# Kernel optimization log

Hardware: AMD Instinct MI355X
Metric: run time of the kernel (lower is better)

## Reference

```python
import jax, jax.numpy as jnp
import numpy as np

EPS = 1e-6
H, HKV, D = 32, 8, 64          # heads, kv heads, head_dim
E, TOP_K, FF = 8, 2, 1024      # experts, top-k, expert intermediate
HID = 2048


def rms_norm(x, w):
    xf = x.astype(jnp.float32)
    var = jnp.mean(xf * xf, axis=-1, keepdims=True)
    return (w * (xf * jax.lax.rsqrt(var + EPS)).astype(x.dtype))


def rotate_half(x):
    x1, x2 = jnp.split(x, 2, axis=-1)
    return jnp.concatenate([-x2, x1], axis=-1)


def apply_rope(q, k, cos, sin):
    # cos/sin: [B,S,rd] -> [B,1,S,rd]
    cos = cos[:, None, :, :]
    sin = sin[:, None, :, :]
    rd = cos.shape[-1]
    q_rot, q_pass = q[..., :rd], q[..., rd:]
    k_rot, k_pass = k[..., :rd], k[..., rd:]
    q_emb = q_rot * cos + rotate_half(q_rot) * sin
    k_emb = k_rot * cos + rotate_half(k_rot) * sin
    return (jnp.concatenate([q_emb, q_pass], -1), jnp.concatenate([k_emb, k_pass], -1))


def attention(x, cos, sin, wq, wk, wv, wo):
    B, S, _ = x.shape
    q = (x @ wq).reshape(B, S, H, D).transpose(0, 2, 1, 3)      # [B,H,S,D]
    k = (x @ wk).reshape(B, S, HKV, D).transpose(0, 2, 1, 3)    # [B,Hk,S,D]
    v = (x @ wv).reshape(B, S, HKV, D).transpose(0, 2, 1, 3)
    q, k = apply_rope(q, k, cos, sin)
    rep = H // HKV
    k = jnp.repeat(k, rep, axis=1)
    v = jnp.repeat(v, rep, axis=1)
    scale = D ** -0.5
    scores = jnp.einsum('bhqd,bhkd->bhqk', q, k) * scale
    causal = jnp.triu(jnp.full((S, S), -jnp.inf, dtype=scores.dtype), k=1)
    scores = scores + causal
    probs = jax.nn.softmax(scores.astype(jnp.float32), axis=-1).astype(q.dtype)
    out = jnp.einsum('bhqk,bhkd->bhqd', probs, v)
    out = out.transpose(0, 2, 1, 3).reshape(B, S, H * D)
    return out @ wo


def moe(x, gate_w, corr_bias, w1, w2, w3):
    B, S, Dm = x.shape
    xf = x.reshape(-1, Dm)                                      # [T, Dm]
    T = xf.shape[0]
    logits = xf @ gate_w                                        # [T, E]
    rw = jax.nn.sigmoid(logits.astype(jnp.float32))
    scores = rw + corr_bias
    _, sel = jax.lax.top_k(scores, TOP_K)                       # [T, k]
    tw = jnp.take_along_axis(rw, sel, axis=-1)
    tw = tw / jnp.sum(tw, axis=-1, keepdims=True)
    # dense [T, E] combine weights (zero for unselected experts)
    cw = jnp.zeros((T, E), dtype=xf.dtype).at[jnp.arange(T)[:, None], sel].set(tw.astype(xf.dtype))
    # run every expert densely, combine with sparse weights (same math as gather/scatter loop)
    h = jax.nn.silu(jnp.einsum('td,edf->etf', xf, w1)) * jnp.einsum('td,edf->etf', xf, w3)
    eo = jnp.einsum('etf,efd->etd', h, w2)                      # [E, T, Dm]
    out = jnp.einsum('etd,te->td', eo, cw)
    return out.reshape(B, S, Dm)


def setup_inputs() -> dict:
    key = jax.random.key(0)
    ks = jax.random.split(key, 16)
    s = 0.02
    return {
        'hidden_states': jax.random.normal(ks[0], (2, 1024, HID), jnp.float32),
        'cos': jax.random.uniform(ks[1], (2, 1024, D), jnp.float32),
        'sin': jax.random.uniform(ks[2], (2, 1024, D), jnp.float32),
        'ln1_w': jnp.ones((HID,), jnp.float32),
        'ln2_w': jnp.ones((HID,), jnp.float32),
        'wq': jax.random.normal(ks[3], (HID, H * D), jnp.float32) * s,
        'wk': jax.random.normal(ks[4], (HID, HKV * D), jnp.float32) * s,
        'wv': jax.random.normal(ks[5], (HID, HKV * D), jnp.float32) * s,
        'wo': jax.random.normal(ks[6], (H * D, HID), jnp.float32) * s,
        'gate_w': jax.random.normal(ks[7], (HID, E), jnp.float32) * s,
        'corr_bias': jnp.zeros((E,), jnp.float32),
        'w1': jax.random.normal(ks[8], (E, HID, FF), jnp.float32) * s,
        'w2': jax.random.normal(ks[9], (E, FF, HID), jnp.float32) * s,
        'w3': jax.random.normal(ks[10], (E, HID, FF), jnp.float32) * s,
    }


def reference(hidden_states, cos, sin, ln1_w, ln2_w, wq, wk, wv, wo, gate_w, corr_bias, w1, w2, w3):
    residual = hidden_states
    h = rms_norm(hidden_states, ln1_w)
    h = attention(h, cos, sin, wq, wk, wv, wo)
    h = residual + h
    residual = h
    h = rms_norm(h, ln2_w)
    h = moe(h, gate_w, corr_bias, w1, w2, w3)
    return residual + h
```

## Files before the change

kernel.cpp:

```cpp
#include <hip/hip_runtime.h>
#include <hip/hip_bf16.h>

#define DEV static __device__ __forceinline__

typedef __attribute__((ext_vector_type(8))) short short8;
typedef __attribute__((ext_vector_type(8))) __bf16 bf16x8;
typedef __attribute__((ext_vector_type(4))) float floatx4;

DEV short f2bf(float f) {
  unsigned u = __builtin_bit_cast(unsigned, f);
  unsigned r = (u + 0x7fffu + ((u >> 16) & 1u)) >> 16;
  return (short)(unsigned short)r;
}
DEV float bf2f(short s) {
  unsigned u = ((unsigned)(unsigned short)s) << 16;
  return __builtin_bit_cast(float, u);
}
DEV floatx4 mfma16(short8 a, short8 b, floatx4 c) {
  return __builtin_amdgcn_mfma_f32_16x16x32_bf16(
      __builtin_bit_cast(bf16x8, a), __builtin_bit_cast(bf16x8, b), c, 0, 0, 0);
}

DEV int sw2(int r) { return (r ^ (r >> 2)) & 3; }

DEV const short* sbase(const short* src, int ld, int row0, int id) {
  int r = id >> 2, cc = id & 3;
  return src + (long)(row0 + r) * ld + ((cc ^ sw2(r)) << 3);
}
DEV void sissue(short* ldsbuf, const short* base, int k0, int tid, int slotbase) {
  int wave = tid >> 6;
  __builtin_amdgcn_global_load_lds(
      (const __attribute__((address_space(1))) void*)(base + k0),
      (__attribute__((address_space(3))) void*)(ldsbuf + (slotbase + wave * 64) * 8),
      16, 0, 0);
}
DEV short8 rdfrag(const short* lds, int row, int l4) {
  return *(const short8*)(lds + row * 32 + ((l4 ^ sw2(row)) << 3));
}

DEV const short* sb64(const short* src, int ld, int row0, int id) {
  int r = id >> 3, c = id & 7;
  return src + (long)(row0 + r) * ld + ((c ^ (r & 7)) << 3);
}
DEV const short* sb64g(const short* src, int ld, const int* rows, int p0, int plim,
                       int id) {
  int r = id >> 3, c = id & 7;
  int pi = p0 + r;
  if (pi > plim) pi = plim;
  return src + (long)rows[pi] * ld + ((c ^ (r & 7)) << 3);
}
DEV short8 rd64(const short* lds, int row, int ch) {
  return *(const short8*)(lds + row * 64 + ((ch ^ (row & 7)) << 3));
}

__global__ __launch_bounds__(256) void k_gemm_qkv(
    const short* Ah, const short* Al, const short* Bh, const short* Bl,
    short* qbh, short* qbl, short* kbh, short* kbl, short* vbh, short* vbl,
    const float* cs, const float* sn) {
  const int K = 2048;
  __shared__ __align__(16) short AsH[2][4096], AsL[2][4096], BsH[2][4096], BsL[2][4096];
  int tid = threadIdx.x, lane = tid & 63, wave = tid >> 6;
  int l15 = lane & 15, l4 = lane >> 4;
  int wm = wave >> 1, wn = wave & 1;
  int bid = blockIdx.y * 24 + blockIdx.x;
  int swz = (bid & 7) * 48 + (bid >> 3);
  int bx = swz % 24, by = swz / 24;
  int m0 = by * 128, n0 = bx * 128;

  const short* bAH0 = sbase(Ah, K, m0, tid);
  const short* bAH1 = sbase(Ah, K, m0, tid + 256);
  const short* bAL0 = sbase(Al, K, m0, tid);
  const short* bAL1 = sbase(Al, K, m0, tid + 256);
  const short* bBH0 = sbase(Bh, K, n0, tid);
  const short* bBH1 = sbase(Bh, K, n0, tid + 256);
  const short* bBL0 = sbase(Bl, K, n0, tid);
  const short* bBL1 = sbase(Bl, K, n0, tid + 256);

  auto STAGE = [&](int buf, int k0) {
    sissue(AsH[buf], bAH0, k0, tid, 0);
    sissue(AsH[buf], bAH1, k0, tid, 256);
    sissue(AsL[buf], bAL0, k0, tid, 0);
    sissue(AsL[buf], bAL1, k0, tid, 256);
    sissue(BsH[buf], bBH0, k0, tid, 0);
    sissue(BsH[buf], bBH1, k0, tid, 256);
    sissue(BsL[buf], bBL0, k0, tid, 0);
    sissue(BsL[buf], bBL1, k0, tid, 256);
  };

  floatx4 zero4 = {0.f, 0.f, 0.f, 0.f};
  floatx4 acc[4][4];
#pragma unroll
  for (int i = 0; i < 4; ++i)
#pragma unroll
    for (int j = 0; j < 4; ++j) acc[i][j] = zero4;

  STAGE(0, 0);
  __syncthreads();
  int cur = 0;
  for (int k0 = 0; k0 < K; k0 += 32) {
    if (k0 + 32 < K) STAGE(cur ^ 1, k0 + 32);
    short8 ah[4], al[4], bh2[4], bl2[4];
#pragma unroll
    for (int mi = 0; mi < 4; ++mi) {
      ah[mi] = rdfrag(AsH[cur], wm * 64 + mi * 16 + l15, l4);
      al[mi] = rdfrag(AsL[cur], wm * 64 + mi * 16 + l15, l4);
    }
#pragma unroll
    for (int nt = 0; nt < 4; ++nt) {
      bh2[nt] = rdfrag(BsH[cur], wn * 64 + nt * 16 + l15, l4);
      bl2[nt] = rdfrag(BsL[cur], wn * 64 + nt * 16 + l15, l4);
    }
#pragma unroll
    for (int mi = 0; mi < 4; ++mi)
#pragma unroll
      for (int nt = 0; nt < 4; ++nt) {
        acc[mi][nt] = mfma16(al[mi], bh2[nt], acc[mi][nt]);
        acc[mi][nt] = mfma16(ah[mi], bl2[nt], acc[mi][nt]);
        acc[mi][nt] = mfma16(ah[mi], bh2[nt], acc[mi][nt]);
      }
    __syncthreads();
    cur ^= 1;
  }

  int hb = n0 + wn * 64;
  bool isq = hb < 2048, isk = (!isq) && hb < 2560;
  if (isq || isk) {
#pragma unroll
    for (int mi = 0; mi < 4; ++mi)
#pragma unroll
      for (int ntp = 0; ntp < 2; ++ntp)
#pragma unroll
        for (int j = 0; j < 4; ++j) {
          int row = m0 + wm * 64 + mi * 16 + l4 * 4 + j;
          int d = ntp * 16 + l15;
          float x0 = acc[mi][ntp][j], x1 = acc[mi][ntp + 2][j];
          float c0 = cs[row * 64 + d], c1 = cs[row * 64 + d + 32];
          float s0 = sn[row * 64 + d], s1 = sn[row * 64 + d + 32];
          float y0 = x0 * c0 - x1 * s0;
          float y1 = x1 * c1 + x0 * s1;
          if (isq) { y0 *= 0.125f; y1 *= 0.125f; }
          acc[mi][ntp][j] = y0;
          acc[mi][ntp + 2][j] = y1;
        }
  }
  short* Ch; short* Cl; int ldc, coff;
  if (isq)      { Ch = qbh; Cl = qbl; ldc = 2048; coff = hb; }
  else if (isk) { Ch = kbh; Cl = kbl; ldc = 512;  coff = hb - 2048; }
  else          { Ch = vbh; Cl = vbl; ldc = 512;  coff = hb - 2560; }
#pragma unroll
  for (int mi = 0; mi < 4; ++mi)
#pragma unroll
    for (int nt = 0; nt < 4; ++nt) {
      int row = m0 + wm * 64 + mi * 16 + l4 * 4;
      int col = coff + nt * 16 + l15;
#pragma unroll
      for (int j = 0; j < 4; ++j) {
        float v = acc[mi][nt][j];
        long ix = (long)(row + j) * ldc + col;
        short hi = f2bf(v);
        Ch[ix] = hi;
        Cl[ix] = f2bf(v - bf2f(hi));
      }
    }
}

__global__ __launch_bounds__(256) void k_gemm_wo(const short* Ah, const short* Al,
                                                 const short* Bh, const short* Bl,
                                                 const float* resid, float* out) {
  const int K = 2048;
  __shared__ __align__(16) short AsH[2][4096], AsL[2][4096], BsH[2][2048], BsL[2][2048];
  int tid = threadIdx.x, lane = tid & 63, wave = tid >> 6;
  int l15 = lane & 15, l4 = lane >> 4;
  int m0 = blockIdx.y * 128, n0 = blockIdx.x * 64;

  const short* bAH0 = sbase(Ah, K, m0, tid);
  const short* bAH1 = sbase(Ah, K, m0, tid + 256);
  const short* bAL0 = sbase(Al, K, m0, tid);
  const short* bAL1 = sbase(Al, K, m0, tid + 256);
  const short* bBH0 = sbase(Bh, K, n0, tid);
  const short* bBL0 = sbase(Bl, K, n0, tid);

  auto STAGE = [&](int buf, int k0) {
    sissue(AsH[buf], bAH0, k0, tid, 0);
    sissue(AsH[buf], bAH1, k0, tid, 256);
    sissue(AsL[buf], bAL0, k0, tid, 0);
    sissue(AsL[buf], bAL1, k0, tid, 256);
    sissue(BsH[buf], bBH0, k0, tid, 0);
    sissue(BsL[buf], bBL0, k0, tid, 0);
  };

  floatx4 zero4 = {0.f, 0.f, 0.f, 0.f};
  floatx4 acc[2][4];
#pragma unroll
  for (int i = 0; i < 2; ++i)
#pragma unroll
    for (int j = 0; j < 4; ++j) acc[i][j] = zero4;

  STAGE(0, 0);
  __syncthreads();
  int cur = 0;
  for (int k0 = 0; k0 < K; k0 += 32) {
    if (k0 + 32 < K) STAGE(cur ^ 1, k0 + 32);
    short8 ah[2], al[2], bh2[4], bl2[4];
#pragma unroll
    for (int mi = 0; mi < 2; ++mi) {
      ah[mi] = rdfrag(AsH[cur], wave * 32 + mi * 16 + l15, l4);
      al[mi] = rdfrag(AsL[cur], wave * 32 + mi * 16 + l15, l4);
    }
#pragma unroll
    for (int nt = 0; nt < 4; ++nt) {
      bh2[nt] = rdfrag(BsH[cur], nt * 16 + l15, l4);
      bl2[nt] = rdfrag(BsL[cur], nt * 16 + l15, l4);
    }
#pragma unroll
    for (int mi = 0; mi < 2; ++mi)
#pragma unroll
      for (int nt = 0; nt < 4; ++nt) {
        acc[mi][nt] = mfma16(al[mi], bh2[nt], acc[mi][nt]);
        acc[mi][nt] = mfma16(ah[mi], bl2[nt], acc[mi][nt]);
        acc[mi][nt] = mfma16(ah[mi], bh2[nt], acc[mi][nt]);
      }
    __syncthreads();
    cur ^= 1;
  }
#pragma unroll
  for (int mi = 0; mi < 2; ++mi)
#pragma unroll
    for (int nt = 0; nt < 4; ++nt) {
      int row = m0 + wave * 32 + mi * 16 + l4 * 4;
      int col = n0 + nt * 16 + l15;
#pragma unroll
      for (int j = 0; j < 4; ++j) {
        long ix = (long)(row + j) * 2048 + col;
        out[ix] = resid[ix] + acc[mi][nt][j];
      }
    }
}

__global__ __launch_bounds__(256) void k_moe_a(const short* X, const short* W1T,
                                               const short* W3T, const int* rows,
                                               const int* cnt, const int* eoff,
                                               short* hh) {
  int e = blockIdx.z;
  int c = cnt[e];
  int mtile = blockIdx.y;
  if (mtile * 128 >= c) return;
  int p0 = eoff[e] + mtile * 128;
  int plim = eoff[e] + c - 1;
  const short* B1 = W1T + (long)e * 1024 * 2048;
  const short* B3 = W3T + (long)e * 1024 * 2048;
  int n0 = blockIdx.x * 64;
  __shared__ __align__(16) short As_[2][8192], B1s[2][4096], B3s[2][4096];
  int tid = threadIdx.x, lane = tid & 63, wave = tid >> 6;
  int l15 = lane & 15, l4 = lane >> 4;
  int wm = wave >> 1, wn = wave & 1;

  const short* bA0 = sb64g(X, 2048, rows, p0, plim, tid);
  const short* bA1 = sb64g(X, 2048, rows, p0, plim, tid + 256);
  const short* bA2 = sb64g(X, 2048, rows, p0, plim, tid + 512);
  const short* bA3 = sb64g(X, 2048, rows, p0, plim, tid + 768);
  const short* bB1_0 = sb64(B1, 2048, n0, tid);
  const short* bB1_1 = sb64(B1, 2048, n0, tid + 256);
  const short* bB3_0 = sb64(B3, 2048, n0, tid);
  const short* bB3_1 = sb64(B3, 2048, n0, tid + 256);

  auto STAGE = [&](int buf, int k0) {
    sissue(As_[buf], bA0, k0, tid, 0);
    sissue(As_[buf], bA1, k0, tid, 256);
    sissue(As_[buf], bA2, k0, tid, 512);
    sissue(As_[buf], bA3, k0, tid, 768);
    sissue(B1s[buf], bB1_0, k0, tid, 0);
    sissue(B1s[buf], bB1_1, k0, tid, 256);
    sissue(B3s[buf], bB3_0, k0, tid, 0);
    sissue(B3s[buf], bB3_1, k0, tid, 256);
  };

  floatx4 zero4 = {0.f, 0.f, 0.f, 0.f};
  floatx4 acc1[4][2], acc3[4][2];
#pragma unroll
  for (int i = 0; i < 4; ++i)
#pragma unroll
    for (int j = 0; j < 2; ++j) { acc1[i][j] = zero4; acc3[i][j] = zero4; }

  STAGE(0, 0);
  __syncthreads();
  int cur = 0;
  for (int k0 = 0; k0 < 2048; k0 += 64) {
    if (k0 + 64 < 2048) STAGE(cur ^ 1, k0 + 64);
#pragma unroll
    for (int kh = 0; kh < 2; ++kh) {
      int ch = kh * 4 + l4;
      short8 af[4], b1f[2], b3f[2];
#pragma unroll
      for (int mi = 0; mi < 4; ++mi)
        af[mi] = rd64(As_[cur], wm * 64 + mi * 16 + l15, ch);
#pragma unroll
      for (int nt = 0; nt < 2; ++nt) {
        b1f[nt] = rd64(B1s[cur], wn * 32 + nt * 16 + l15, ch);
        b3f[nt] = rd64(B3s[cur], wn * 32 + nt * 16 + l15, ch);
      }
#pragma unroll
      for (int mi = 0; mi < 4; ++mi)
#pragma unroll
        for (int nt = 0; nt < 2; ++nt) {
          acc1[mi][nt] = mfma16(af[mi], b1f[nt], acc1[mi][nt]);
          acc3[mi][nt] = mfma16(af[mi], b3f[nt], acc3[mi][nt]);
        }
    }
    __syncthreads();
    cur ^= 1;
  }
#pragma unroll
  for (int mi = 0; mi < 4; ++mi)
#pragma unroll
    for (int nt = 0; nt < 2; ++nt) {
      int col = n0 + wn * 32 + nt * 16 + l15;
#pragma unroll
      for (int j = 0; j < 4; ++j) {
        int rl = wm * 64 + mi * 16 + l4 * 4 + j;
        if (mtile * 128 + rl < c) {
          float v1 = acc1[mi][nt][j], v3 = acc3[mi][nt][j];
          float hg = v1 / (1.f + __expf(-v1));
          hh[(long)(p0 + rl) * 1024 + col] = f2bf(hg * v3);
        }
      }
    }
}

__global__ __launch_bounds__(256) void k_moe_b(const short* hh, const short* W2T,
                                               const int* cnt, const int* eoff,
                                               short* mo) {
  int e = blockIdx.z;
  int c = cnt[e];
  int mtile = blockIdx.y;
  if (mtile * 128 >= c) return;
  int p0 = eoff[e] + mtile * 128;
  const short* B = W2T + (long)e * 2048 * 1024;
  int n0 = blockIdx.x * 128;
  __shared__ __align__(16) short As_[2][8192], Bs_[2][8192];
  int tid = threadIdx.x, lane = tid & 63, wave = tid >> 6;
  int l15 = lane & 15, l4 = lane >> 4;
  int wm = wave >> 1, wn = wave & 1;

  const short* bA0 = sb64(hh, 1024, p0, tid);
  const short* bA1 = sb64(hh, 1024, p0, tid + 256);
  const short* bA2 = sb64(hh, 1024, p0, tid + 512);
  const short* bA3 = sb64(hh, 1024, p0, tid + 768);
  const short* bB0 = sb64(B, 1024, n0, tid);
  const short* bB1 = sb64(B, 1024, n0, tid + 256);
  const short* bB2 = sb64(B, 1024, n0, tid + 512);
  const short* bB3 = sb64(B, 1024, n0, tid + 768);

  auto STAGE = [&](int buf, int k0) {
    sissue(As_[buf], bA0, k0, tid, 0);
    sissue(As_[buf], bA1, k0, tid, 256);
    sissue(As_[buf], bA2, k0, tid, 512);
    sissue(As_[buf], bA3, k0, tid, 768);
    sissue(Bs_[buf], bB0, k0, tid, 0);
    sissue(Bs_[buf], bB1, k0, tid, 256);
    sissue(Bs_[buf], bB2, k0, tid, 512);
    sissue(Bs_[buf], bB3, k0, tid, 768);
  };

  floatx4 zero4 = {0.f, 0.f, 0.f, 0.f};
  floatx4 acc[4][4];
#pragma unroll
  for (int i = 0; i < 4; ++i)
#pragma unroll
    for (int j = 0; j < 4; ++j) acc[i][j] = zero4;

  STAGE(0, 0);
  __syncthreads();
  int cur = 0;
  for (int k0 = 0; k0 < 1024; k0 += 64) {
    if (k0 + 64 < 1024) STAGE(cur ^ 1, k0 + 64);
#pragma unroll
    for (int kh = 0; kh < 2; ++kh) {
      int ch = kh * 4 + l4;
      short8 af[4], bfv[4];
#pragma unroll
      for (int mi = 0; mi < 4; ++mi)
        af[mi] = rd64(As_[cur], wm * 64 + mi * 16 + l15, ch);
#pragma unroll
      for (int nt = 0; nt < 4; ++nt)
        bfv[nt] = rd64(Bs_[cur], wn * 64 + nt * 16 + l15, ch);
#pragma unroll
      for (int mi = 0; mi < 4; ++mi)
#pragma unroll
        for (int nt = 0; nt < 4; ++nt)
          acc[mi][nt] = mfma16(af[mi], bfv[nt], acc[mi][nt]);
    }
    __syncthreads();
    cur ^= 1;
  }
#pragma unroll
  for (int mi = 0; mi < 4; ++mi)
#pragma unroll
    for (int nt = 0; nt < 4; ++nt) {
      int col = n0 + wn * 64 + nt * 16 + l15;
#pragma unroll
      for (int j = 0; j < 4; ++j) {
        int rl = wm * 64 + mi * 16 + l4 * 4 + j;
        if (mtile * 128 + rl < c) mo[(long)(p0 + rl) * 2048 + col] = f2bf(acc[mi][nt][j]);
      }
    }
}

__global__ __launch_bounds__(256) void k_transv(const short* vbh, const short* vbl,
                                                short* vth, short* vtl) {
  __shared__ __align__(16) short th[64][72], tl[64][72];
  int tt = blockIdx.x;
  int bk = blockIdx.y;
  int b = bk >> 3, kvh = bk & 7;
  int tid = threadIdx.x;
#pragma unroll
  for (int it = 0; it < 2; ++it) {
    int id = it * 256 + tid;
    int r = id >> 3, cc = id & 7;
    long src = (long)(b * 1024 + tt * 64 + r) * 512 + kvh * 64 + cc * 8;
    *(uint4*)(&th[r][cc * 8]) = *(const uint4*)(vbh + src);
    *(uint4*)(&tl[r][cc * 8]) = *(const uint4*)(vbl + src);
  }
  __syncthreads();
#pragma unroll
  for (int it = 0; it < 2; ++it) {
    int id = it * 256 + tid;
    int n = id >> 3, kc = id & 7;
    short8 oh2, ol2;
#pragma unroll
    for (int j = 0; j < 8; ++j) { oh2[j] = th[kc * 8 + j][n]; ol2[j] = tl[kc * 8 + j][n]; }
    long dst = (long)bk * 65536 + (long)n * 1024 + tt * 64 + kc * 8;
    *(short8*)(vth + dst) = oh2;
    *(short8*)(vtl + dst) = ol2;
  }
}

DEV int vsw(int r) { return (r ^ (r >> 3)) & 7; }
DEV short8 avread(const short* buf, int row, int c) {
  return *(const short8*)(buf + row * 64 + (((c ^ vsw(row)) & 7) << 3));
}
DEV int aswz(int r, int c) { return r * 64 + (((c ^ ((r ^ (r >> 3)) & 7)) & 7) << 3); }
DEV void glds(short* ldsslot, const short* src) {
  __builtin_amdgcn_global_load_lds(
      (const __attribute__((address_space(1))) void*)src,
      (__attribute__((address_space(3))) void*)ldsslot, 16, 0, 0);
}

__global__ __launch_bounds__(256) void k_attn3(
    const short* qhp, const short* qlp, const short* khp, const short* klp,
    const short* vth2, const short* vtl2, short* oh, short* ol) {
  int xp = blockIdx.x, bh = blockIdx.y;
  int h = bh & 31, b = bh >> 5, kvh = h >> 2;
  int tid = threadIdx.x, wave = tid >> 6, lane = tid & 63;
  int l15 = lane & 15, l4 = lane >> 4;
  int qtA = 15 - xp, qtB = xp;

  __shared__ __align__(16) short Kh[2][4096], Kl[2][4096], Vh[2][4096], Vl[2][4096];
  __shared__ __align__(16) short Ph[4][1024], Pl[4][1024];

  short8 qh[2][2], ql[2][2];
#pragma unroll
  for (int tt = 0; tt < 2; ++tt) {
    int qrow = (tt ? qtB : qtA) * 64 + wave * 16 + l15;
    long qoff = ((long)(b * 1024 + qrow)) * 2048 + h * 64;
    qh[tt][0] = *(const short8*)(qhp + qoff + l4 * 8);
    qh[tt][1] = *(const short8*)(qhp + qoff + 32 + l4 * 8);
    ql[tt][0] = *(const short8*)(qlp + qoff + l4 * 8);
    ql[tt][1] = *(const short8*)(qlp + qoff + 32 + l4 * 8);
  }

  floatx4 zero4 = {0.f, 0.f, 0.f, 0.f};
  floatx4 acco[2][4];
  float mrun[2][4], lrun[2][4];
#pragma unroll
  for (int tt = 0; tt < 2; ++tt)
#pragma unroll
    for (int j = 0; j < 4; ++j) {
      acco[tt][j] = zero4;
      mrun[tt][j] = -1e30f;
      lrun[tt][j] = 0.f;
    }

  const short* khb = khp + ((long)b * 1024) * 512 + kvh * 64;
  const short* klb = klp + ((long)b * 1024) * 512 + kvh * 64;
  const short* vhb = vth2 + (long)(b * 8 + kvh) * 65536;
  const short* vlb = vtl2 + (long)(b * 8 + kvh) * 65536;

  int r0 = tid >> 3, c0 = tid & 7;
  int r1 = r0 + 32;
  const short* kh0 = khb + (long)r0 * 512 + ((c0 ^ vsw(r0)) << 3);
  const short* kh1 = khb + (long)r1 * 512 + ((c0 ^ vsw(r1)) << 3);
  const short* kl0 = klb + (long)r0 * 512 + ((c0 ^ vsw(r0)) << 3);
  const short* kl1 = klb + (long)r1 * 512 + ((c0 ^ vsw(r1)) << 3);
  const short* vh0 = vhb + (long)r0 * 1024 + ((c0 ^ vsw(r0)) << 3);
  const short* vh1 = vhb + (long)r1 * 1024 + ((c0 ^ vsw(r1)) << 3);
  const short* vl0 = vlb + (long)r0 * 1024 + ((c0 ^ vsw(r0)) << 3);
  const short* vl1 = vlb + (long)r1 * 1024 + ((c0 ^ vsw(r1)) << 3);
  int wslot = wave * 512;

  auto STAGE = [&](int buf, int kt) {
    int ko = kt * 32768;
    int vo = kt * 64;
    glds(&Kh[buf][wslot], kh0 + ko);
    glds(&Kh[buf][2048 + wslot], kh1 + ko);
    glds(&Kl[buf][wslot], kl0 + ko);
    glds(&Kl[buf][2048 + wslot], kl1 + ko);
    glds(&Vh[buf][wslot], vh0 + vo);
    glds(&Vh[buf][2048 + wslot], vh1 + vo);
    glds(&Vl[buf][wslot], vl0 + vo);
    glds(&Vl[buf][2048 + wslot], vl1 + vo);
  };

  STAGE(0, 0);
  int cur = 0;
  for (int kt = 0; kt <= qtA; ++kt) {
    __syncthreads();
    if (kt < qtA) STAGE(cur ^ 1, kt + 1);
#pragma unroll
    for (int tt = 0; tt < 2; ++tt) {
      int qtt = tt ? qtB : qtA;
      if (tt == 1 && kt > qtB) continue;
      floatx4 accs[4] = {zero4, zero4, zero4, zero4};
#pragma unroll
      for (int ks = 0; ks < 2; ++ks) {
        short8 qah = qh[tt][ks];
        short8 qal = ql[tt][ks];
#pragma unroll
        for (int nt = 0; nt < 4; ++nt) {
          int kvr = nt * 16 + l15;
          short8 kfh = avread(Kh[cur], kvr, l4 + 4 * ks);
          short8 kfl = avread(Kl[cur], kvr, l4 + 4 * ks);
          accs[nt] = mfma16(qal, kfh, accs[nt]);
          accs[nt] = mfma16(qah, kfl, accs[nt]);
          accs[nt] = mfma16(qah, kfh, accs[nt]);
        }
      }
      if (kt == qtt) {
#pragma unroll
        for (int nt = 0; nt < 4; ++nt)
#pragma unroll
          for (int j = 0; j < 4; ++j) {
            int kvg = nt * 16 + l15;
            int qg = wave * 16 + l4 * 4 + j;
            if (kvg > qg) accs[nt][j] = -1e30f;
          }
      }
      float pj[4][4];
#pragma unroll
      for (int j = 0; j < 4; ++j) {
        float mx = fmaxf(fmaxf(accs[0][j], accs[1][j]), fmaxf(accs[2][j], accs[3][j]));
        mx = fmaxf(mx, __shfl_xor(mx, 1));
        mx = fmaxf(mx, __shfl_xor(mx, 2));
        mx = fmaxf(mx, __shfl_xor(mx, 4));
        mx = fmaxf(mx, __shfl_xor(mx, 8));
        float mnew = fmaxf(mrun[tt][j], mx);
        float alpha = __expf(mrun[tt][j] - mnew);
        float rs = 0.f;
#pragma unroll
        for (int nt = 0; nt < 4; ++nt) {
          float pv = __expf(accs[nt][j] - mnew);
          pj[nt][j] = pv;
          rs += pv;
        }
        rs += __shfl_xor(rs, 1);
        rs += __shfl_xor(rs, 2);
        rs += __shfl_xor(rs, 4);
        rs += __shfl_xor(rs, 8);
        lrun[tt][j] = lrun[tt][j] * alpha + rs;
        mrun[tt][j] = mnew;
        acco[tt][0][j] *= alpha; acco[tt][1][j] *= alpha;
        acco[tt][2][j] *= alpha; acco[tt][3][j] *= alpha;
      }
      short* P = Ph[wave];
      short* P2 = Pl[wave];
#pragma unroll
      for (int nt = 0; nt < 4; ++nt)
#pragma unroll
        for (int j = 0; j < 4; ++j) {
          int rr = l4 * 4 + j, col = nt * 16 + l15;
          float pv = pj[nt][j];
          short hi = f2bf(pv);
          int ad = aswz(rr, col >> 3) + (col & 7);
          P[ad] = hi;
          P2[ad] = f2bf(pv - bf2f(hi));
        }
      asm volatile("s_waitcnt lgkmcnt(0)" ::: "memory");
      __builtin_amdgcn_sched_barrier(0);
#pragma unroll
      for (int ks = 0; ks < 2; ++ks) {
        short8 pah = *(const short8*)(P + aswz(l15, l4 + 4 * ks));
        short8 pal = *(const short8*)(P2 + aswz(l15, l4 + 4 * ks));
#pragma unroll
        for (int nt = 0; nt < 4; ++nt) {
          int dr = nt * 16 + l15;
          short8 vfh = avread(Vh[cur], dr, l4 + 4 * ks);
          short8 vfl = avread(Vl[cur], dr, l4 + 4 * ks);
          acco[tt][nt] = mfma16(pal, vfh, acco[tt][nt]);
          acco[tt][nt] = mfma16(pah, vfl, acco[tt][nt]);
          acco[tt][nt] = mfma16(pah, vfh, acco[tt][nt]);
        }
      }
    }
    cur ^= 1;
  }
#pragma unroll
  for (int tt = 0; tt < 2; ++tt) {
    int qtt = tt ? qtB : qtA;
#pragma unroll
    for (int j = 0; j < 4; ++j) {
      float invl = 1.f / lrun[tt][j];
      int qg = qtt * 64 + wave * 16 + l4 * 4 + j;
      long ooff = ((long)(b * 1024 + qg)) * 2048 + h * 64;
#pragma unroll
      for (int nt = 0; nt < 4; ++nt) {
        float v = acco[tt][nt][j] * invl;
        short hi = f2bf(v);
        oh[ooff + nt * 16 + l15] = hi;
        ol[ooff + nt * 16 + l15] = f2bf(v - bf2f(hi));
      }
    }
  }
}

DEV void trans_load(const float* src, int N, int n0, int k0, float (*t)[65], int tid) {
  int r = tid >> 2, cq = tid & 3;
  const float* s = src + (long)(k0 + r) * N + n0 + cq * 16;
#pragma unroll
  for (int i = 0; i < 4; ++i) {
    float4 v = *(const float4*)(s + i * 4);
    t[r][cq * 16 + i * 4 + 0] = v.x;
    t[r][cq * 16 + i * 4 + 1] = v.y;
    t[r][cq * 16 + i * 4 + 2] = v.z;
    t[r][cq * 16 + i * 4 + 3] = v.w;
  }
}

DEV void trans_tile1(const float* src, short* dst, int N, int K, int n0, int k0,
                     float (*t)[65]) {
  int tid = threadIdx.x;
  trans_load(src, N, n0, k0, t, tid);
  __syncthreads();
  int n = tid >> 2, kc = tid & 3;
#pragma unroll
  for (int ii = 0; ii < 2; ++ii) {
    short8 o;
#pragma unroll
    for (int j = 0; j < 8; ++j) o[j] = f2bf(t[kc * 16 + ii * 8 + j][n]);
    *(short8*)(dst + (long)(n0 + n) * K + k0 + kc * 16 + ii * 8) = o;
  }
}

DEV void trans_tile2(const float* src, short* dh, short* dl, int N, int K, int n0,
                     int k0, float (*t)[65]) {
  int tid = threadIdx.x;
  trans_load(src, N, n0, k0, t, tid);
  __syncthreads();
  int n = tid >> 2, kc = tid & 3;
#pragma unroll
  for (int ii = 0; ii < 2; ++ii) {
    short8 ohv, olv;
#pragma unroll
    for (int j = 0; j < 8; ++j) {
      float v = t[kc * 16 + ii * 8 + j][n];
      short hi = f2bf(v);
      ohv[j] = hi;
      olv[j] = f2bf(v - bf2f(hi));
    }
    *(short8*)(dh + (long)(n0 + n) * K + k0 + kc * 16 + ii * 8) = ohv;
    *(short8*)(dl + (long)(n0 + n) * K + k0 + kc * 16 + ii * 8) = olv;
  }
}

__global__ __launch_bounds__(256) void k_trans_attn(
    const float* wq, const float* wk, const float* wv, const float* wo,
    short* qkvTh, short* qkvTl, short* woTh, short* woTl) {
  __shared__ float t[64][65];
  int x = blockIdx.x, kt = blockIdx.y;
  const float* src; short* dh; short* dl; int N, n0;
  if (x < 32)      { src = wq; dh = qkvTh; dl = qkvTl; N = 2048; n0 = x * 64; }
  else if (x < 40) { src = wk; dh = qkvTh + 2048L * 2048; dl = qkvTl + 2048L * 2048;
                     N = 512; n0 = (x - 32) * 64; }
  else if (x < 48) { src = wv; dh = qkvTh + 2560L * 2048; dl = qkvTl + 2560L * 2048;
                     N = 512; n0 = (x - 40) * 64; }
  else             { src = wo; dh = woTh; dl = woTl; N = 2048; n0 = (x - 48) * 64; }
  trans_tile2(src, dh, dl, N, 2048, n0, kt * 64, t);
}

__global__ __launch_bounds__(256) void k_trans_moe13(const float* w1, const float* w3,
                                                     short* w1T, short* w3T) {
  __shared__ float t[64][65];
  int x = blockIdx.x, kt = blockIdx.y;
  const float* src; short* dst; int n0;
  if (x < 128) { int e = x >> 4; src = w1 + (long)e * 2048 * 1024;
                 dst = w1T + (long)e * 1024 * 2048; n0 = (x & 15) * 64; }
  else         { int i = x - 128, e = i >> 4; src = w3 + (long)e * 2048 * 1024;
                 dst = w3T + (long)e * 1024 * 2048; n0 = (i & 15) * 64; }
  trans_tile1(src, dst, 1024, 2048, n0, kt * 64, t);
}

__global__ __launch_bounds__(256) void k_trans_w2(const float* w2, short* w2T) {
  __shared__ float t[64][65];
  int e = blockIdx.x >> 5, ntb = blockIdx.x & 31, kt = blockIdx.y;
  trans_tile1(w2 + (long)e * 1024 * 2048, w2T + (long)e * 2048 * 1024,
              2048, 1024, ntb * 64, kt * 64, t);
}

__global__ __launch_bounds__(256) void k_rmsnorm1(const float* x, const float* w,
                                                  short* outh, short* outl) {
  int row = blockIdx.x, tid = threadIdx.x;
  const float* xr = x + (long)row * 2048;
  float4 a = *(const float4*)(xr + tid * 8);
  float4 c = *(const float4*)(xr + tid * 8 + 4);
  float ss = a.x * a.x + a.y * a.y + a.z * a.z + a.w * a.w +
             c.x * c.x + c.y * c.y + c.z * c.z + c.w * c.w;
  ss += __shfl_xor(ss, 1);  ss += __shfl_xor(ss, 2);  ss += __shfl_xor(ss, 4);
  ss += __shfl_xor(ss, 8);  ss += __shfl_xor(ss, 16); ss += __shfl_xor(ss, 32);
  __shared__ float red[4];
  int wave = tid >> 6;
  if ((tid & 63) == 0) red[wave] = ss;
  __syncthreads();
  float tot = red[0] + red[1] + red[2] + red[3];
  float inv = 1.f / sqrtf(tot * (1.f / 2048.f) + 1e-6f);
  float4 w0 = *(const float4*)(w + tid * 8);
  float4 w1 = *(const float4*)(w + tid * 8 + 4);
  float xv[8] = {a.x * w0.x, a.y * w0.y, a.z * w0.z, a.w * w0.w,
                 c.x * w1.x, c.y * w1.y, c.z * w1.z, c.w * w1.w};
  short8 ohv, olv;
#pragma unroll
  for (int j = 0; j < 8; ++j) {
    float v = xv[j] * inv;
    short hi = f2bf(v);
    ohv[j] = hi;
    olv[j] = f2bf(v - bf2f(hi));
  }
  *(short8*)(outh + (long)row * 2048 + tid * 8) = ohv;
  *(short8*)(outl + (long)row * 2048 + tid * 8) = olv;
}

__global__ __launch_bounds__(256) void k_rmsnorm2_gate(const float* x, const float* w,
                                                       const float* gw, const float* cb,
                                                       short* out, int* sel, float* tw,
                                                       int* cnt) {
  int row = blockIdx.x, tid = threadIdx.x;
  const float* xr = x + (long)row * 2048;
  float4 a = *(const float4*)(xr + tid * 8);
  float4 c = *(const float4*)(xr + tid * 8 + 4);
  float ss = a.x * a.x + a.y * a.y + a.z * a.z + a.w * a.w +
             c.x * c.x + c.y * c.y + c.z * c.z + c.w * c.w;
  ss += __shfl_xor(ss, 1);  ss += __shfl_xor(ss, 2);  ss += __shfl_xor(ss, 4);
  ss += __shfl_xor(ss, 8);  ss += __shfl_xor(ss, 16); ss += __shfl_xor(ss, 32);
  __shared__ float red[4];
  int wave = tid >> 6;
  if ((tid & 63) == 0) red[wave] = ss;
  __syncthreads();
  float tot = red[0] + red[1] + red[2] + red[3];
  float inv = 1.f / sqrtf(tot * (1.f / 2048.f) + 1e-6f);
  float4 w0 = *(const float4*)(w + tid * 8);
  float4 w1 = *(const float4*)(w + tid * 8 + 4);
  float xn[8];
  xn[0] = a.x * inv * w0.x; xn[1] = a.y * inv * w0.y; xn[2] = a.z * inv * w0.z;
  xn[3] = a.w * inv * w0.w; xn[4] = c.x * inv * w1.x; xn[5] = c.y * inv * w1.y;
  xn[6] = c.z * inv * w1.z; xn[7] = c.w * inv * w1.w;
  short8 o;
#pragma unroll
  for (int j = 0; j < 8; ++j) o[j] = f2bf(xn[j]);
  *(short8*)(out + (long)row * 2048 + tid * 8) = o;
  float gp[8] = {0.f, 0.f, 0.f, 0.f, 0.f, 0.f, 0.f, 0.f};
#pragma unroll
  for (int j = 0; j < 8; ++j) {
    const float* g = gw + (long)(tid * 8 + j) * 8;
    float4 g0 = *(const float4*)g;
    float4 g1 = *(const float4*)(g + 4);
    gp[0] += xn[j] * g0.x; gp[1] += xn[j] * g0.y; gp[2] += xn[j] * g0.z; gp[3] += xn[j] * g0.w;
    gp[4] += xn[j] * g1.x; gp[5] += xn[j] * g1.y; gp[6] += xn[j] * g1.z; gp[7] += xn[j] * g1.w;
  }
#pragma unroll
  for (int e = 0; e < 8; ++e) {
    gp[e] += __shfl_xor(gp[e], 1);  gp[e] += __shfl_xor(gp[e], 2);
    gp[e] += __shfl_xor(gp[e], 4);  gp[e] += __shfl_xor(gp[e], 8);
    gp[e] += __shfl_xor(gp[e], 16); gp[e] += __shfl_xor(gp[e], 32);
  }
  __shared__ float gred[4][8];
  __shared__ float srw[8], ssc[8];
  if ((tid & 63) == 0) {
#pragma unroll
    for (int e = 0; e < 8; ++e) gred[wave][e] = gp[e];
  }
  __syncthreads();
  if (tid < 8) {
    float lg = gred[0][tid] + gred[1][tid] + gred[2][tid] + gred[3][tid];
    float rw = 1.f / (1.f + expf(-lg));
    srw[tid] = rw;
    ssc[tid] = rw + cb[tid];
  }
  __syncthreads();
  if (tid == 0) {
    int e0 = 0; float b0 = ssc[0];
    for (int e = 1; e < 8; ++e) if (ssc[e] > b0) { b0 = ssc[e]; e0 = e; }
    int e1 = -1; float b1 = -1e30f;
    for (int e = 0; e < 8; ++e) if (e != e0 && ssc[e] > b1) { b1 = ssc[e]; e1 = e; }
    float t0 = srw[e0], t1 = srw[e1], s = t0 + t1;
    sel[row * 2] = e0; sel[row * 2 + 1] = e1;
    tw[row * 2] = t0 / s; tw[row * 2 + 1] = t1 / s;
    atomicAdd(&cnt[e0], 1);
    atomicAdd(&cnt[e1], 1);
  }
}

__global__ void k_scan(const int* cnt, int* eoff) {
  if (threadIdx.x == 0) {
    int s = 0;
    for (int e = 0; e < 8; ++e) { eoff[e] = s; s += cnt[e]; }
  }
}

__global__ __launch_bounds__(256) void k_scatter(const int* sel, const int* eoff,
                                                 int* fill, int* rows, int* pos) {
  int t = blockIdx.x * 256 + threadIdx.x;
  if (t >= 2048) return;
  for (int k = 0; k < 2; ++k) {
    int e = sel[t * 2 + k];
    int p = eoff[e] + atomicAdd(&fill[e], 1);
    rows[p] = t;
    pos[t * 2 + k] = p;
  }
}

__global__ __launch_bounds__(256) void k_combine(float* out, const short* mo,
                                                 const int* pos, const float* tw) {
  int t = blockIdx.x, tid = threadIdx.x;
  int p0 = pos[t * 2], p1 = pos[t * 2 + 1];
  float w0 = tw[t * 2], w1 = tw[t * 2 + 1];
  float* o = out + (long)t * 2048 + tid * 8;
  short8 m0 = *(const short8*)(mo + (long)p0 * 2048 + tid * 8);
  short8 m1 = *(const short8*)(mo + (long)p1 * 2048 + tid * 8);
  float4 a = *(const float4*)o;
  float4 b = *(const float4*)(o + 4);
  a.x += w0 * bf2f(m0[0]) + w1 * bf2f(m1[0]);
  a.y += w0 * bf2f(m0[1]) + w1 * bf2f(m1[1]);
  a.z += w0 * bf2f(m0[2]) + w1 * bf2f(m1[2]);
  a.w += w0 * bf2f(m0[3]) + w1 * bf2f(m1[3]);
  b.x += w0 * bf2f(m0[4]) + w1 * bf2f(m1[4]);
  b.y += w0 * bf2f(m0[5]) + w1 * bf2f(m1[5]);
  b.z += w0 * bf2f(m0[6]) + w1 * bf2f(m1[6]);
  b.w += w0 * bf2f(m0[7]) + w1 * bf2f(m1[7]);
  *(float4*)o = a;
  *(float4*)(o + 4) = b;
}

extern "C" void kernel_launch(void* const* d_in, const int* in_sizes, int n_in,
                              void* d_out, int out_size, void* d_ws, size_t ws_size,
                              hipStream_t stream) {
  const float* x    = (const float*)d_in[0];
  const float* cosb = (const float*)d_in[1];
  const float* sinb = (const float*)d_in[2];
  const float* ln1  = (const float*)d_in[3];
  const float* ln2  = (const float*)d_in[4];
  const float* wq   = (const float*)d_in[5];
  const float* wk   = (const float*)d_in[6];
  const float* wv   = (const float*)d_in[7];
  const float* wo   = (const float*)d_in[8];
  const float* gw   = (const float*)d_in[9];
  const float* cb   = (const float*)d_in[10];
  const float* w1   = (const float*)d_in[11];
  const float* w2   = (const float*)d_in[12];
  const float* w3   = (const float*)d_in[13];
  float* out = (float*)d_out;

  char* p = (char*)d_ws;
  auto take = [&](size_t n) { char* r = p; p += (n + 255) & ~(size_t)255; return r; };
  short* qkvTh = (short*)take(3072L * 2048 * 2);
  short* qkvTl = (short*)take(3072L * 2048 * 2);
  short* woTh  = (short*)take(2048L * 2048 * 2);
  short* woTl  = (short*)take(2048L * 2048 * 2);
  short* w1T   = (short*)take(8L * 1024 * 2048 * 2);
  short* w3T   = (short*)take(8L * 1024 * 2048 * 2);
  short* w2T   = (short*)take(8L * 2048 * 1024 * 2);
  short* hbh   = (short*)take(2048L * 2048 * 2);
  short* hbl   = (short*)take(2048L * 2048 * 2);
  short* qbh   = (short*)take(2048L * 2048 * 2);
  short* qbl   = (short*)take(2048L * 2048 * 2);
  short* kbh   = (short*)take(2048L * 512 * 2);
  short* kbl   = (short*)take(2048L * 512 * 2);
  short* vbh   = (short*)take(2048L * 512 * 2);
  short* vbl   = (short*)take(2048L * 512 * 2);
  short* vth   = (short*)take(16L * 64 * 1024 * 2);
  short* vtl   = (short*)take(16L * 64 * 1024 * 2);
  short* aoh   = (short*)take(2048L * 2048 * 2);
  short* aol   = (short*)take(2048L * 2048 * 2);
  short* h2b   = (short*)take(2048L * 2048 * 2);
  short* hhb   = (short*)take(4224L * 1024 * 2);
  short* mob   = (short*)take(4352L * 2048 * 2);
  int* rti     = (int*)take(64 * sizeof(int));
  int* cnt = rti; int* fill = rti + 8; int* eoff = rti + 16;
  int* sel     = (int*)take(2048L * 2 * 4);
  float* twb   = (float*)take(2048L * 2 * 4);
  int* rowsp   = (int*)take(4352L * 4);
  int* posb    = (int*)take(2048L * 2 * 4);
  (void)ws_size; (void)in_sizes; (void)n_in; (void)out_size;

  dim3 B256(256);
  k_trans_attn<<<dim3(80, 32), B256, 0, stream>>>(wq, wk, wv, wo, qkvTh, qkvTl,
                                                  woTh, woTl);
  k_trans_moe13<<<dim3(256, 32), B256, 0, stream>>>(w1, w3, w1T, w3T);
  k_trans_w2<<<dim3(256, 16), B256, 0, stream>>>(w2, w2T);
  hipMemsetAsync(rti, 0, 64, stream);

  k_rmsnorm1<<<dim3(2048), B256, 0, stream>>>(x, ln1, hbh, hbl);
  k_gemm_qkv<<<dim3(24, 16), B256, 0, stream>>>(hbh, hbl, qkvTh, qkvTl, qbh, qbl,
                                                kbh, kbl, vbh, vbl, cosb, sinb);
  k_transv<<<dim3(16, 16), B256, 0, stream>>>(vbh, vbl, vth, vtl);
  k_attn3<<<dim3(8, 64), B256, 0, stream>>>(qbh, qbl, kbh, kbl, vth, vtl, aoh, aol);
  k_gemm_wo<<<dim3(32, 16), B256, 0, stream>>>(aoh, aol, woTh, woTl, x, out);

  k_rmsnorm2_gate<<<dim3(2048), B256, 0, stream>>>(out, ln2, gw, cb, h2b, sel, twb, cnt);
  k_scan<<<dim3(1), dim3(64), 0, stream>>>(cnt, eoff);
  k_scatter<<<dim3(8), B256, 0, stream>>>(sel, eoff, fill, rowsp, posb);
  k_moe_a<<<dim3(16, 16, 8), B256, 0, stream>>>(h2b, w1T, w3T, rowsp, cnt, eoff, hhb);
  k_moe_b<<<dim3(16, 16, 8), B256, 0, stream>>>(hhb, w2T, cnt, eoff, mob);
  k_combine<<<dim3(2048), B256, 0, stream>>>(out, mob, posb, twb);
}
```

Measured before the change: 561.5 us.

## Keep two global-to-LDS stages in flight with explicit vmcnt waits in GEMM loops

All four GEMM kernels (QKV+RoPE, output projection, MoE up/gate, MoE down) now prefetch two K-stages up front. Each iteration waits with a partial s_waitcnt vmcnt, so only the current buffer's loads must land while the next stage's loads stay outstanding. The refill of the buffer just consumed is issued after the end-of-iteration barrier. This replaces __syncthreads, which drains all outstanding loads, to hide more global memory latency. The hand-counted vmcnt values must match the number of loads each STAGE issues per thread, or the kernels will read stale LDS data.

```diff
diff --git a/kernel.cpp b/kernel.cpp
--- a/kernel.cpp
+++ b/kernel.cpp
@@ -20,6 +20,9 @@
   return __builtin_amdgcn_mfma_f32_16x16x32_bf16(
       __builtin_bit_cast(bf16x8, a), __builtin_bit_cast(bf16x8, b), c, 0, 0, 0);
 }
+
+#define VMCNT(n) asm volatile("s_waitcnt vmcnt(" #n ")" ::: "memory")
+#define SBAR() __builtin_amdgcn_s_barrier()
 
 DEV int sw2(int r) { return (r ^ (r >> 2)) & 3; }
 
@@ -95,10 +98,11 @@
     for (int j = 0; j < 4; ++j) acc[i][j] = zero4;
 
   STAGE(0, 0);
-  __syncthreads();
+  STAGE(1, 32);
   int cur = 0;
   for (int k0 = 0; k0 < K; k0 += 32) {
-    if (k0 + 32 < K) STAGE(cur ^ 1, k0 + 32);
+    if (k0 + 64 < K) VMCNT(8); else VMCNT(0);
+    SBAR();
     short8 ah[4], al[4], bh2[4], bl2[4];
 #pragma unroll
     for (int mi = 0; mi < 4; ++mi) {
@@ -118,7 +122,8 @@
         acc[mi][nt] = mfma16(ah[mi], bl2[nt], acc[mi][nt]);
         acc[mi][nt] = mfma16(ah[mi], bh2[nt], acc[mi][nt]);
       }
-    __syncthreads();
+    SBAR();
+    if (k0 + 64 < K) STAGE(cur, k0 + 64);
     cur ^= 1;
   }
 
@@ -197,10 +202,11 @@
     for (int j = 0; j < 4; ++j) acc[i][j] = zero4;
 
   STAGE(0, 0);
-  __syncthreads();
+  STAGE(1, 32);
   int cur = 0;
   for (int k0 = 0; k0 < K; k0 += 32) {
-    if (k0 + 32 < K) STAGE(cur ^ 1, k0 + 32);
+    if (k0 + 64 < K) VMCNT(6); else VMCNT(0);
+    SBAR();
     short8 ah[2], al[2], bh2[4], bl2[4];
 #pragma unroll
     for (int mi = 0; mi < 2; ++mi) {
@@ -220,7 +226,8 @@
         acc[mi][nt] = mfma16(ah[mi], bl2[nt], acc[mi][nt]);
         acc[mi][nt] = mfma16(ah[mi], bh2[nt], acc[mi][nt]);
       }
-    __syncthreads();
+    SBAR();
+    if (k0 + 64 < K) STAGE(cur, k0 + 64);
     cur ^= 1;
   }
 #pragma unroll
@@ -283,10 +290,11 @@
     for (int j = 0; j < 2; ++j) { acc1[i][j] = zero4; acc3[i][j] = zero4; }
 
   STAGE(0, 0);
-  __syncthreads();
+  STAGE(1, 64);
   int cur = 0;
   for (int k0 = 0; k0 < 2048; k0 += 64) {
-    if (k0 + 64 < 2048) STAGE(cur ^ 1, k0 + 64);
+    if (k0 + 128 < 2048) VMCNT(8); else VMCNT(0);
+    SBAR();
 #pragma unroll
     for (int kh = 0; kh < 2; ++kh) {
       int ch = kh * 4 + l4;
@@ -307,7 +315,8 @@
           acc3[mi][nt] = mfma16(af[mi], b3f[nt], acc3[mi][nt]);
         }
     }
-    __syncthreads();
+    SBAR();
+    if (k0 + 128 < 2048) STAGE(cur, k0 + 128);
     cur ^= 1;
   }
 #pragma unroll
@@ -370,10 +379,11 @@
     for (int j = 0; j < 4; ++j) acc[i][j] = zero4;
 
   STAGE(0, 0);
-  __syncthreads();
+  STAGE(1, 64);
   int cur = 0;
   for (int k0 = 0; k0 < 1024; k0 += 64) {
-    if (k0 + 64 < 1024) STAGE(cur ^ 1, k0 + 64);
+    if (k0 + 128 < 1024) VMCNT(8); else VMCNT(0);
+    SBAR();
 #pragma unroll
     for (int kh = 0; kh < 2; ++kh) {
       int ch = kh * 4 + l4;
@@ -390,7 +400,8 @@
         for (int nt = 0; nt < 4; ++nt)
           acc[mi][nt] = mfma16(af[mi], bfv[nt], acc[mi][nt]);
     }
-    __syncthreads();
+    SBAR();
+    if (k0 + 128 < 1024) STAGE(cur, k0 + 128);
     cur ^= 1;
   }
 #pragma unroll
```

After: 550.9 us. About the same (-1.9%).
